# Kernel tuning notes

Hardware: AMD Instinct MI355X
Metric: run time of the kernel (lower is better)

## Reference

```python
import jax, jax.numpy as jnp
import numpy as np
import math

HEAD_SIZE = 64
WINDOW = 512  # sliding_window_size


def setup_inputs() -> dict:
    key = jax.random.key(0)
    k1, k2, k3, k4 = jax.random.split(key, 4)
    B, T, C = 4, 4096, 1024
    x = jax.random.normal(k1, (B, T, C), dtype=jnp.float32)
    # torch nn.Linear(C, head_size, bias=False) computes x @ W.T with W [hs, C];
    # we store the transposed [C, hs] layout so projection is x @ w.
    s = 1.0 / math.sqrt(C)
    w_key = jax.random.uniform(k2, (C, HEAD_SIZE), jnp.float32, -s, s)
    w_query = jax.random.uniform(k3, (C, HEAD_SIZE), jnp.float32, -s, s)
    w_value = jax.random.uniform(k4, (C, HEAD_SIZE), jnp.float32, -s, s)
    return {"x": x, "w_key": w_key, "w_query": w_query, "w_value": w_value}


def reference(x, w_key, w_query, w_value):
    # Non-cache path (use_cache=False): keys/values are the fresh projections,
    # q_start = k_start = 0, win_size = sliding_window_size.
    B, T, C = x.shape
    q = x @ w_query          # [B, T, hs]
    k = x @ w_key            # [B, T, hs]
    v = x @ w_value          # [B, T, hs]

    # attn_scores = q @ k^T  -> [B, T, T]
    scores = jnp.einsum('btd,bsd->bts', q, k)

    # Sliding-window causal mask: invalid where diff < 0 or diff >= window,
    # with diff = q_pos - k_pos.
    pos = jnp.arange(T)
    diff = pos[:, None] - pos[None, :]          # [T, T]
    mask_bool = (diff < 0) | (diff >= WINDOW)

    scale = math.sqrt(HEAD_SIZE)
    scores = jnp.where(mask_bool[None, :, :], -jnp.inf, scores)
    attn = jax.nn.softmax(scores / scale, axis=-1)  # dropout p=0.0 -> identity

    out = jnp.einsum('bts,bsd->btd', attn, v)   # [B, T, hs]
    return out
```

## Files before the change

### kernel.cpp

```cpp
#include <hip/hip_runtime.h>
#include <hip/hip_bf16.h>
#include <math.h>

#define BB 4
#define TT 4096
#define CC 1024
#define HS 64
#define WIN 512
#define NROW (BB*TT)

typedef float f32x4 __attribute__((ext_vector_type(4)));
typedef short bf16x8 __attribute__((ext_vector_type(8)));

#define MFMA16(a, b, c) __builtin_amdgcn_mfma_f32_16x16x32_bf16((a), (b), (c), 0, 0, 0)

#define GLOAD_LDS(gp, lp) __builtin_amdgcn_global_load_lds( \
    (const __attribute__((address_space(1))) void*)(gp), \
    (__attribute__((address_space(3))) void*)(lp), 16, 0, 0)

__device__ inline unsigned short f2b(float f) {
  union { __hip_bfloat16 h; unsigned short u; } v;
  v.h = __float2bfloat16(f);
  return v.u;
}

__global__ __launch_bounds__(256) void pack_w_kernel(
    const float* __restrict__ wq, const float* __restrict__ wk,
    const float* __restrict__ wv, unsigned short* __restrict__ wp)
{
  int t = blockIdx.x * 256 + threadIdx.x;
  int kg = t / 48;
  int nq = t % 48;
  int n0 = nq * 4;
  int m  = n0 >> 6;
  int c  = n0 & 63;
  const float* w = (m == 0) ? wq : (m == 1) ? wk : wv;
  float4 v = *(const float4*)&w[(size_t)kg * HS + c];
  int kt = kg >> 5;
  int hi = (kg >> 3) & 3;
  int j  = kg & 7;
  float vals[4] = {v.x, v.y, v.z, v.w};
  #pragma unroll
  for (int i = 0; i < 4; ++i) {
    int n  = n0 + i;
    int nb = n >> 4;
    int rl = n & 15;
    int lane = hi * 16 + rl;
    wp[((size_t)(kt * 12 + nb) * 64 + lane) * 8 + j] = f2b(vals[i]);
  }
}

__global__ __launch_bounds__(256) void proj_mfma_kernel(
    const float* __restrict__ x, const unsigned short* __restrict__ wp,
    unsigned short* __restrict__ q_ws, unsigned short* __restrict__ k_ws,
    unsigned short* __restrict__ vt_ws)
{
  __shared__ unsigned char xbuf[2][8192];
  __shared__ unsigned char wbuf[2][24576];

  const int tid = threadIdx.x;
  const int l   = tid & 63;
  const int cq  = tid >> 6;
  const int rl  = l & 15;
  const int hi  = l >> 4;
  const int r0  = blockIdx.x * 32;

  f32x4 acc[2][3];
  #pragma unroll
  for (int g = 0; g < 2; ++g)
    #pragma unroll
    for (int j = 0; j < 3; ++j) acc[g][j] = (f32x4){0.f, 0.f, 0.f, 0.f};

#define STAGE(KS, BUF) { \
    _Pragma("unroll") \
    for (int r = 0; r < 2; ++r) { \
      int s  = r * 256 + tid; \
      int h2 = s & 1; \
      int lq = (s >> 1) & 63; \
      int f  = s >> 7; \
      int row = r0 + (f & 1) * 16 + (lq & 15); \
      int col = (KS) * 64 + (f >> 1) * 32 + (lq >> 4) * 8 + h2 * 4; \
      GLOAD_LDS(x + (size_t)row * CC + col, &xbuf[BUF][s * 16]); \
    } \
    const unsigned short* wsrc = wp + (size_t)(KS) * 12288; \
    _Pragma("unroll") \
    for (int r = 0; r < 6; ++r) { \
      int t = r * 256 + tid; \
      GLOAD_LDS(wsrc + t * 8, &wbuf[BUF][t * 16]); \
    } }

  STAGE(0, 0)
  asm volatile("s_waitcnt vmcnt(0)" ::: "memory");
  __syncthreads();

  for (int ks = 0; ks < 16; ++ks) {
    const int cur = ks & 1;
    if (ks < 15) STAGE(ks + 1, cur ^ 1)

    #pragma unroll
    for (int ktl = 0; ktl < 2; ++ktl) {
      bf16x8 afr[2];
      #pragma unroll
      for (int g = 0; g < 2; ++g) {
        const float* ap = (const float*)&xbuf[cur][(((ktl * 2 + g) * 64 + l) * 32)];
        f32x4 a0 = *(const f32x4*)ap;
        f32x4 a1 = *(const f32x4*)(ap + 4);
        bf16x8 af;
        af[0] = (short)f2b(a0[0]); af[1] = (short)f2b(a0[1]);
        af[2] = (short)f2b(a0[2]); af[3] = (short)f2b(a0[3]);
        af[4] = (short)f2b(a1[0]); af[5] = (short)f2b(a1[1]);
        af[6] = (short)f2b(a1[2]); af[7] = (short)f2b(a1[3]);
        afr[g] = af;
      }
      #pragma unroll
      for (int j = 0; j < 3; ++j) {
        bf16x8 wf = *(const bf16x8*)&wbuf[cur][((ktl * 12 + cq * 3 + j) * 64 + l) * 16];
        acc[0][j] = MFMA16(afr[0], wf, acc[0][j]);
        acc[1][j] = MFMA16(afr[1], wf, acc[1][j]);
      }
    }

    asm volatile("s_waitcnt vmcnt(0)" ::: "memory");
    __syncthreads();
  }
#undef STAGE

  #pragma unroll
  for (int g = 0; g < 2; ++g) {
    int rb = r0 + g * 16;
    #pragma unroll
    for (int j = 0; j < 3; ++j) {
      int nb = cq * 3 + j;
      if (nb < 8) {
        unsigned short* dst = (nb < 4) ? q_ws : k_ws;
        int c = (nb & 3) * 16 + rl;
        #pragma unroll
        for (int r = 0; r < 4; ++r) {
          int row = rb + hi * 4 + r;
          dst[(size_t)row * HS + c] = f2b(acc[g][j][r]);
        }
      } else {
        int ch   = rb >> 6;
        int key0 = (rb & 63) + hi * 4;
        int d = (nb - 8) * 16 + rl;
        unsigned u0 = (unsigned)f2b(acc[g][j][0]) | ((unsigned)f2b(acc[g][j][1]) << 16);
        unsigned u1 = (unsigned)f2b(acc[g][j][2]) | ((unsigned)f2b(acc[g][j][3]) << 16);
        uint2 uu; uu.x = u0; uu.y = u1;
        *(uint2*)(vt_ws + (size_t)ch * 4096 + d * 64 + key0) = uu;
      }
    }
  }
}

__global__ __launch_bounds__(256) void attn_mfma_kernel(
    const unsigned short* __restrict__ q_ws, const unsigned short* __restrict__ k_ws,
    const unsigned short* __restrict__ vt_ws, float* __restrict__ out)
{
  __shared__ uint4 smem4[1600];
  unsigned char* smem = (unsigned char*)smem4;

  const int tid = threadIdx.x;
  const int l   = tid & 63;
  const int wid = tid >> 6;
  const int rl  = l & 15;
  const int hi  = l >> 4;
  const int b   = blockIdx.x >> 6;
  const int qt  = blockIdx.x & 63;
  const int t0  = qt * 64;
  const int t0w = t0 + wid * 16;

  const unsigned short* qrow = q_ws + (size_t)(b * TT + t0w + rl) * HS;
  bf16x8 qb0 = *(const bf16x8*)(qrow + hi * 8);
  bf16x8 qb1 = *(const bf16x8*)(qrow + 32 + hi * 8);

  f32x4 oacc[4];
  #pragma unroll
  for (int i = 0; i < 4; ++i) oacc[i] = (f32x4){0.f, 0.f, 0.f, 0.f};
  float m_run = -INFINITY, l_run = 0.f;

  int s_lo = t0 - WIN; if (s_lo < 0) s_lo = 0;
  unsigned char* pbase = smem + 16384 + wid * 2304 + rl * 144;

  for (int sc = s_lo; sc < t0 + 64; sc += 64) {
    __syncthreads();
    {
      const unsigned short* kg = k_ws + (size_t)(b * TT + sc) * HS;
      const unsigned short* vg = vt_ws + (size_t)((b * TT + sc) >> 6) * 4096;
      #pragma unroll
      for (int i = 0; i < 2; ++i) {
        int idx = tid + i * 256;
        int row = idx >> 3;
        int c16 = idx & 7;
        uint4 kv = *(const uint4*)(kg + row * 64 + c16 * 8);
        uint4 vv = *(const uint4*)(vg + row * 64 + c16 * 8);
        *(uint4*)(smem + row * 128 + ((c16 ^ (row & 7)) * 16)) = kv;
        *(uint4*)(smem + 8192 + row * 128 + ((c16 ^ (row & 7)) * 16)) = vv;
      }
    }
    __syncthreads();

    f32x4 sacc[4];
    #pragma unroll
    for (int i = 0; i < 4; ++i) sacc[i] = (f32x4){0.f, 0.f, 0.f, 0.f};
    #pragma unroll
    for (int kb = 0; kb < 4; ++kb) {
      int row = kb * 16 + rl;
      unsigned char* kr = smem + row * 128;
      bf16x8 k0 = *(const bf16x8*)(kr + (((hi) ^ (row & 7)) * 16));
      bf16x8 k1 = *(const bf16x8*)(kr + (((4 + hi) ^ (row & 7)) * 16));
      sacc[kb] = MFMA16(k0, qb0, sacc[kb]);
      sacc[kb] = MFMA16(k1, qb1, sacc[kb]);
    }

    const int tg = t0w + rl;
    float p[16];
    float tm = -INFINITY;
    bool full = (sc + 63 <= t0w) && (sc >= t0w - 496);
    #pragma unroll
    for (int kb = 0; kb < 4; ++kb)
      #pragma unroll
      for (int r = 0; r < 4; ++r) {
        float v = sacc[kb][r] * 0.125f;
        if (!full) {
          int key = sc + kb * 16 + hi * 4 + r;
          int diff = tg - key;
          v = (diff >= 0 && diff < WIN) ? v : -INFINITY;
        }
        p[kb * 4 + r] = v;
        tm = fmaxf(tm, v);
      }
    tm = fmaxf(tm, __shfl_xor(tm, 16));
    tm = fmaxf(tm, __shfl_xor(tm, 32));
    float m_new = fmaxf(m_run, tm);
    float fac  = (m_new == -INFINITY) ? 1.f : __expf(m_run - m_new);
    float msub = (m_new == -INFINITY) ? 0.f : m_new;
    float lsum = 0.f;
    #pragma unroll
    for (int i = 0; i < 16; ++i) { p[i] = __expf(p[i] - msub); lsum += p[i]; }
    lsum += __shfl_xor(lsum, 16);
    lsum += __shfl_xor(lsum, 32);
    l_run = l_run * fac + lsum;
    m_run = m_new;

    #pragma unroll
    for (int kb = 0; kb < 4; ++kb) {
      unsigned u0 = (unsigned)f2b(p[kb * 4 + 0]) | ((unsigned)f2b(p[kb * 4 + 1]) << 16);
      unsigned u1 = (unsigned)f2b(p[kb * 4 + 2]) | ((unsigned)f2b(p[kb * 4 + 3]) << 16);
      uint2 uu; uu.x = u0; uu.y = u1;
      *(uint2*)(pbase + kb * 32 + hi * 8) = uu;
    }

    #pragma unroll
    for (int r = 0; r < 4; ++r) {
      float fr = __shfl(fac, (l & 48) | (hi * 4 + r));
      oacc[0][r] *= fr; oacc[1][r] *= fr; oacc[2][r] *= fr; oacc[3][r] *= fr;
    }

    bf16x8 pa0 = *(const bf16x8*)(pbase + hi * 16);
    bf16x8 pa1 = *(const bf16x8*)(pbase + 64 + hi * 16);
    #pragma unroll
    for (int f = 0; f < 4; ++f) {
      int d = f * 16 + rl;
      unsigned char* vr = smem + 8192 + d * 128;
      bf16x8 v0 = *(const bf16x8*)(vr + (((hi) ^ (d & 7)) * 16));
      bf16x8 v1 = *(const bf16x8*)(vr + (((4 + hi) ^ (d & 7)) * 16));
      oacc[f] = MFMA16(pa0, v0, oacc[f]);
      oacc[f] = MFMA16(pa1, v1, oacc[f]);
    }
  }

  float inv = 1.f / l_run;
  #pragma unroll
  for (int r = 0; r < 4; ++r) {
    float ir = __shfl(inv, (l & 48) | (hi * 4 + r));
    int row = b * TT + t0w + hi * 4 + r;
    #pragma unroll
    for (int f = 0; f < 4; ++f)
      out[(size_t)row * HS + f * 16 + rl] = oacc[f][r] * ir;
  }
}

extern "C" void kernel_launch(void* const* d_in, const int* in_sizes, int n_in,
                              void* d_out, int out_size, void* d_ws, size_t ws_size,
                              hipStream_t stream) {
  const float* x  = (const float*)d_in[0];
  const float* wk = (const float*)d_in[1];
  const float* wq = (const float*)d_in[2];
  const float* wv = (const float*)d_in[3];
  float* out = (float*)d_out;

  unsigned short* wp    = (unsigned short*)d_ws;
  unsigned short* q_ws  = wp + 196608;
  unsigned short* k_ws  = q_ws + (size_t)NROW * HS;
  unsigned short* vt_ws = k_ws + (size_t)NROW * HS;

  pack_w_kernel<<<192, 256, 0, stream>>>(wq, wk, wv, wp);
  proj_mfma_kernel<<<NROW / 32, 256, 0, stream>>>(x, wp, q_ws, k_ws, vt_ws);
  attn_mfma_kernel<<<BB * (TT / 64), 256, 0, stream>>>(q_ws, k_ws, vt_ws, out);
}
```

Baseline: 47.13 us.

## Load projection weights to registers and triple-buffer swizzled x tiles in LDS

The projection kernel no longer stages weight fragments through LDS. Each wave now loads its weight fragments straight into registers, with two register sets alternating across k-steps. The x tile is kept in a triple-buffered LDS ring with an XOR swizzle, so reads are meant to avoid bank conflicts. Fixed vmcnt waits and sched barriers let the next stages load while the current one computes. This cuts LDS traffic and footprint, at the cost of more registers and fragile hand-counted wait thresholds.

```diff
diff --git a/kernel.cpp b/kernel.cpp
--- a/kernel.cpp
+++ b/kernel.cpp
@@ -55,8 +55,7 @@
     unsigned short* __restrict__ q_ws, unsigned short* __restrict__ k_ws,
     unsigned short* __restrict__ vt_ws)
 {
-  __shared__ unsigned char xbuf[2][8192];
-  __shared__ unsigned char wbuf[2][24576];
+  __shared__ unsigned char xbuf[3][8192];
 
   const int tid = threadIdx.x;
   const int l   = tid & 63;
@@ -71,59 +70,88 @@
     #pragma unroll
     for (int j = 0; j < 3; ++j) acc[g][j] = (f32x4){0.f, 0.f, 0.f, 0.f};
 
-#define STAGE(KS, BUF) { \
+#define SX(KS, BUF) { \
     _Pragma("unroll") \
     for (int r = 0; r < 2; ++r) { \
-      int s  = r * 256 + tid; \
-      int h2 = s & 1; \
-      int lq = (s >> 1) & 63; \
-      int f  = s >> 7; \
-      int row = r0 + (f & 1) * 16 + (lq & 15); \
-      int col = (KS) * 64 + (f >> 1) * 32 + (lq >> 4) * 8 + h2 * 4; \
-      GLOAD_LDS(x + (size_t)row * CC + col, &xbuf[BUF][s * 16]); \
-    } \
-    const unsigned short* wsrc = wp + (size_t)(KS) * 12288; \
+      int s    = r * 256 + tid; \
+      int row  = s >> 4; \
+      int cpos = s & 15; \
+      int cg   = cpos ^ ((row & 7) << 1); \
+      GLOAD_LDS(x + (size_t)(r0 + row) * CC + (KS) * 64 + cg * 4, \
+                &xbuf[BUF][s * 16]); \
+    } }
+
+#define LW(KS, WD) { \
     _Pragma("unroll") \
-    for (int r = 0; r < 6; ++r) { \
-      int t = r * 256 + tid; \
-      GLOAD_LDS(wsrc + t * 8, &wbuf[BUF][t * 16]); \
+    for (int ktl = 0; ktl < 2; ++ktl) \
+      _Pragma("unroll") \
+      for (int j = 0; j < 3; ++j) \
+        WD[ktl][j] = *(const bf16x8*)(wp + \
+            ((size_t)((KS) * 24 + ktl * 12 + cq * 3 + j) * 64 + l) * 8); }
+
+#define COMP(BUF, WD) { \
+    _Pragma("unroll") \
+    for (int ktl = 0; ktl < 2; ++ktl) { \
+      bf16x8 afr[2]; \
+      _Pragma("unroll") \
+      for (int g = 0; g < 2; ++g) { \
+        int row = g * 16 + rl; \
+        int sw  = (row & 7) << 1; \
+        int c0  = ktl * 8 + hi * 2; \
+        const unsigned char* rb = &xbuf[BUF][row * 256]; \
+        f32x4 a0 = *(const f32x4*)(rb + ((c0 ^ sw) * 16)); \
+        f32x4 a1 = *(const f32x4*)(rb + (((c0 + 1) ^ sw) * 16)); \
+        bf16x8 af; \
+        af[0] = (short)f2b(a0[0]); af[1] = (short)f2b(a0[1]); \
+        af[2] = (short)f2b(a0[2]); af[3] = (short)f2b(a0[3]); \
+        af[4] = (short)f2b(a1[0]); af[5] = (short)f2b(a1[1]); \
+        af[6] = (short)f2b(a1[2]); af[7] = (short)f2b(a1[3]); \
+        afr[g] = af; \
+      } \
+      _Pragma("unroll") \
+      for (int j = 0; j < 3; ++j) { \
+        acc[0][j] = MFMA16(afr[0], WD[ktl][j], acc[0][j]); \
+        acc[1][j] = MFMA16(afr[1], WD[ktl][j], acc[1][j]); \
+      } \
     } }
 
-  STAGE(0, 0)
-  asm volatile("s_waitcnt vmcnt(0)" ::: "memory");
-  __syncthreads();
-
-  for (int ks = 0; ks < 16; ++ks) {
-    const int cur = ks & 1;
-    if (ks < 15) STAGE(ks + 1, cur ^ 1)
-
-    #pragma unroll
-    for (int ktl = 0; ktl < 2; ++ktl) {
-      bf16x8 afr[2];
-      #pragma unroll
-      for (int g = 0; g < 2; ++g) {
-        const float* ap = (const float*)&xbuf[cur][(((ktl * 2 + g) * 64 + l) * 32)];
-        f32x4 a0 = *(const f32x4*)ap;
-        f32x4 a1 = *(const f32x4*)(ap + 4);
-        bf16x8 af;
-        af[0] = (short)f2b(a0[0]); af[1] = (short)f2b(a0[1]);
-        af[2] = (short)f2b(a0[2]); af[3] = (short)f2b(a0[3]);
-        af[4] = (short)f2b(a1[0]); af[5] = (short)f2b(a1[1]);
-        af[6] = (short)f2b(a1[2]); af[7] = (short)f2b(a1[3]);
-        afr[g] = af;
-      }
-      #pragma unroll
-      for (int j = 0; j < 3; ++j) {
-        bf16x8 wf = *(const bf16x8*)&wbuf[cur][((ktl * 12 + cq * 3 + j) * 64 + l) * 16];
-        acc[0][j] = MFMA16(afr[0], wf, acc[0][j]);
-        acc[1][j] = MFMA16(afr[1], wf, acc[1][j]);
-      }
-    }
-
-    asm volatile("s_waitcnt vmcnt(0)" ::: "memory");
-    __syncthreads();
-  }
-#undef STAGE
+#define PHASE_WAIT(N) { \
+    asm volatile("s_waitcnt vmcnt(" #N ")" ::: "memory"); \
+    __builtin_amdgcn_sched_barrier(0); \
+    __builtin_amdgcn_s_barrier(); }
+
+#define PHASE_END { \
+    asm volatile("s_waitcnt lgkmcnt(0)" ::: "memory"); \
+    __builtin_amdgcn_sched_barrier(0); \
+    __builtin_amdgcn_s_barrier(); }
+
+  bf16x8 wA[2][3], wB[2][3];
+
+  SX(0, 0) SX(1, 1) SX(2, 2)
+  LW(0, wA) LW(1, wB)
+
+  #pragma unroll 1
+  for (int ks = 0; ks < 16; ks += 2) {
+    const int bufA = ks % 3;
+    const int bufB = (ks + 1) % 3;
+    PHASE_WAIT(6)
+    COMP(bufA, wA)
+    PHASE_END
+    if (ks + 3 <= 15) { SX(ks + 3, (ks + 3) % 3) }
+    if (ks + 2 <= 15) { LW(ks + 2, wA) }
+    __builtin_amdgcn_sched_barrier(0);
+    if (ks + 1 < 15) { PHASE_WAIT(6) } else { PHASE_WAIT(0) }
+    COMP(bufB, wB)
+    PHASE_END
+    if (ks + 4 <= 15) { SX(ks + 4, (ks + 4) % 3) }
+    if (ks + 3 <= 15) { LW(ks + 3, wB) }
+    __builtin_amdgcn_sched_barrier(0);
+  }
+#undef SX
+#undef LW
+#undef COMP
+#undef PHASE_WAIT
+#undef PHASE_END
 
   #pragma unroll
   for (int g = 0; g < 2; ++g) {
```

Result: faster. 45.56 us (-3.3%).
